# Performance work log

Hardware: AMD Instinct MI355X
Metric: run time of the kernel (lower is better)

## Reference

```python
import jax, jax.numpy as jnp
import numpy as np

DIM = 512
HEADS = 8
DIM_HEAD = 64
BLOCKS = 6
EXCHANGES = 3
EPS = 1.1920929e-07  # torch.finfo(float32).eps used by RMSNorm(eps=None)


def _rmsnorm(x, w):
    return x * jax.lax.rsqrt(jnp.mean(x * x, axis=-1, keepdims=True) + EPS) * w


def _attention(x, ctx, nw, wq, wkv, wo):
    # x: [B, i, d] queries; ctx: [B, j, d] context (NOT normalized, as in original)
    B = x.shape[0]
    xn = _rmsnorm(x, nw)
    q = jnp.einsum('bid,ed->bie', xn, wq)
    kv = jnp.einsum('bjd,ed->bje', ctx, wkv)
    k, v = jnp.split(kv, 2, axis=-1)
    heads = lambda t: t.reshape(B, t.shape[1], HEADS, DIM_HEAD).transpose(0, 2, 1, 3)
    q, k, v = heads(q), heads(k), heads(v)
    sim = jnp.einsum('bhid,bhjd->bhij', q, k)  # NOTE: original never applies self.scale
    attn = jax.nn.softmax(sim, axis=-1)
    out = jnp.einsum('bhij,bhjd->bhid', attn, v)
    out = out.transpose(0, 2, 1, 3).reshape(B, -1, HEADS * DIM_HEAD)
    return jnp.einsum('bie,de->bid', out, wo)


def _feedforward(x, nw, kw, kb, vw, vb):
    q = _rmsnorm(x, nw)
    h = jnp.einsum('...d,ed->...e', q, kw) + kb
    sim, gates = jnp.split(h, 2, axis=-1)
    h = sim * jax.nn.gelu(gates, approximate=False)  # F.gelu default = exact erf
    return jnp.einsum('...e,de->...d', h, vw) + vb


def _forward(tokens, attn_norm_w, attn_wq, attn_wkv, attn_wo,
             ff_norm_w, ff_keys_w, ff_keys_b, ff_values_w, ff_values_b,
             res_norm_w, res_wq, res_wkv, res_wo):
    b, n, d = tokens.shape
    tokens = jnp.broadcast_to(tokens[None], (BLOCKS, b, n, d))
    messages = [tokens]
    for _ in range(EXCHANGES):
        flat = tokens.reshape(BLOCKS * b, n, d)
        attended = _attention(flat, flat, attn_norm_w, attn_wq, attn_wkv, attn_wo)
        attended = attended.reshape(BLOCKS, b, n, d)
        retrieved = _feedforward(tokens, ff_norm_w, ff_keys_w, ff_keys_b, ff_values_w, ff_values_b)
        messages += [attended, retrieved]
        packed = jnp.concatenate(messages, axis=0)           # [M, b, n, d]
        M = packed.shape[0]
        # einops: repeat 'm b n d -> (b blocks) n m d'
        ctx = jnp.broadcast_to(packed.transpose(1, 2, 0, 3)[:, None], (b, BLOCKS, n, M, d))
        ctx = ctx.reshape(b * BLOCKS * n, M, d)
        # queries packed '(blocks b) n d' then '* n d' -> [blocks*b*n, 1, d]
        q = tokens.reshape(BLOCKS * b * n, 1, d)
        pooled = _attention(q, ctx, res_norm_w, res_wq, res_wkv, res_wo)
        tokens = pooled.reshape(BLOCKS, b, n, d)
    return tokens


def setup_inputs() -> dict:
    key = jax.random.key(0)
    ks = jax.random.split(key, 12)
    b, n, d = 2, 256, DIM
    di = HEADS * DIM_HEAD
    dff = int(d * 4.0 * 2 / 3)
    s = lambda k, shp, fan: (jax.random.normal(k, shp, jnp.float32) / np.sqrt(fan)).astype(jnp.float32)
    return {
        'tokens': jax.random.normal(ks[0], (b, n, d), jnp.float32),
        'attn_norm_w': 1.0 + 0.05 * jax.random.normal(ks[1], (d,), jnp.float32),
        'attn_wq': s(ks[2], (di, d), d),
        'attn_wkv': s(ks[3], (2 * di, d), d),
        'attn_wo': s(ks[4], (d, di), di),
        'ff_norm_w': 1.0 + 0.05 * jax.random.normal(ks[5], (d,), jnp.float32),
        'ff_keys_w': s(ks[6], (2 * dff, d), d),
        'ff_keys_b': 0.01 * jax.random.normal(ks[7], (2 * dff,), jnp.float32),
        'ff_values_w': s(ks[8], (d, dff), dff),
        'ff_values_b': 0.01 * jax.random.normal(ks[9], (d,), jnp.float32),
        'res_norm_w': 1.0 + 0.05 * jax.random.normal(ks[10], (d,), jnp.float32),
        'res_wq': s(ks[11], (di, d), d),
        'res_wkv': s(jax.random.fold_in(key, 100), (2 * di, d), d),
        'res_wo': s(jax.random.fold_in(key, 101), (d, di), di),
    }


def reference(tokens, attn_norm_w, attn_wq, attn_wkv, attn_wo,
              ff_norm_w, ff_keys_w, ff_keys_b, ff_values_w, ff_values_b,
              res_norm_w, res_wq, res_wkv, res_wo):
    return _forward(tokens, attn_norm_w, attn_wq, attn_wkv, attn_wo,
                    ff_norm_w, ff_keys_w, ff_keys_b, ff_values_w, ff_values_b,
                    res_norm_w, res_wq, res_wkv, res_wo)
```

## Files before the change

kernel.cpp:

```cpp
#include <hip/hip_runtime.h>
#include <math.h>

#define Dm   512
#define Nn_  256
#define Bv   2
#define NTD  1024
#define NH   8
#define DH   64
#define DFF  1365
#define DFF2 2730
#define KFF  1408
#define NFF  2816
#define NMD  14
#define EPSR 1.1920929e-07f

typedef _Float16 h16;
typedef h16  v8h  __attribute__((ext_vector_type(8)));
typedef float v4f __attribute__((ext_vector_type(4)));

__device__ inline h16 f2h(float v) { return (h16)v; }

__device__ inline void glds16(const void* g, void* l) {
    __builtin_amdgcn_global_load_lds((const __attribute__((address_space(1))) void*)g,
                                     (__attribute__((address_space(3))) void*)l, 16, 0, 0);
}

struct GDesc {
    const h16* A;
    const h16* W;
    const float* bias;
    const float* rss;
    float* C;
    h16* Cbf;
    long Apl, Wpl, bfpl;
    int lda, ldw, ldc, Nd, mbase, K, mode, nbx;
};

template <int BM, int BN>
__global__ __launch_bounds__(256) void mega_gemm(GDesc d0, GDesc d1, GDesc d2, GDesc d3,
                                                 int n0, int n01, int n012)
{
    constexpr int NWN = (BN == 128) ? 2 : 1;
    constexpr int NWM = 4 / NWN;
    constexpr int MI = BM / (16 * NWM);
    constexpr int ABUF = BM * 32;
    constexpr int WBUFh = BN * 32;
    constexpr int BUF = 2 * ABUF + 2 * WBUFh;
    constexpr int ASEG = BM / 16;
    constexpr int WSEG = BN / 16;
    constexpr int NSEG = 2 * ASEG + 2 * WSEG;
    __shared__ h16 lds[2 * BUF];

    GDesc d; int lb = blockIdx.x;
    if (lb < n0) d = d0;
    else if (lb < n01) { d = d1; lb -= n0; }
    else if (lb < n012) { d = d2; lb -= n01; }
    else { d = d3; lb -= n012; }
    const int bx = lb % d.nbx;
    const int by = lb / d.nbx;

    const int tid = threadIdx.x;
    const int wid = tid >> 6;
    const int lane = tid & 63;
    const int wm = wid / NWN, wn = wid % NWN;
    const int row16 = lane & 15, quad = lane >> 4;
    const long i0 = (long)bx * BM;
    const long j0 = (long)by * BN;
    const int l4 = lane >> 2;
    const int l2s = ((lane & 3) ^ (l4 & 3)) * 8;
    const int ksw = (quad ^ (row16 & 3)) * 8;

    auto stage = [&](int k0, h16* buf) {
        #pragma unroll
        for (int s = 0; s < NSEG / 4; ++s) {
            const int sg = wid * (NSEG / 4) + s;
            const h16* src;
            int dst;
            if (sg < ASEG) {
                src = d.A + (i0 + sg * 16 + l4) * (long)d.lda + k0 + l2s;
                dst = sg * 512;
            } else if (sg < 2 * ASEG) {
                const int r = sg - ASEG;
                src = d.A + d.Apl + (i0 + r * 16 + l4) * (long)d.lda + k0 + l2s;
                dst = ABUF + r * 512;
            } else if (sg < 2 * ASEG + WSEG) {
                const int r = sg - 2 * ASEG;
                src = d.W + (j0 + r * 16 + l4) * (long)d.ldw + k0 + l2s;
                dst = 2 * ABUF + r * 512;
            } else {
                const int r = sg - 2 * ASEG - WSEG;
                src = d.W + d.Wpl + (j0 + r * 16 + l4) * (long)d.ldw + k0 + l2s;
                dst = 2 * ABUF + WBUFh + r * 512;
            }
            glds16(src, &buf[dst]);
        }
    };

    v4f acc[MI][4];
    #pragma unroll
    for (int a = 0; a < MI; ++a)
        #pragma unroll
        for (int b = 0; b < 4; ++b) acc[a][b] = (v4f){0.f, 0.f, 0.f, 0.f};

    stage(0, lds);
    int cur = 0;
    for (int k0 = 0; k0 < d.K; k0 += 32) {
        __syncthreads();
        h16* cbuf = &lds[cur * BUF];
        if (k0 + 32 < d.K) stage(k0 + 32, &lds[(cur ^ 1) * BUF]);

        v8h af[MI], al[MI];
        #pragma unroll
        for (int mi = 0; mi < MI; ++mi) {
            const int aoff = (wm * (16 * MI) + mi * 16 + row16) * 32 + ksw;
            af[mi] = *(const v8h*)&cbuf[aoff];
            al[mi] = *(const v8h*)&cbuf[ABUF + aoff];
        }
        #pragma unroll
        for (int nj = 0; nj < 4; ++nj) {
            const int boff = (wn * 64 + nj * 16 + row16) * 32 + ksw;
            v8h bh = *(const v8h*)&cbuf[2 * ABUF + boff];
            v8h bl = *(const v8h*)&cbuf[2 * ABUF + WBUFh + boff];
            #pragma unroll
            for (int mi = 0; mi < MI; ++mi) {
                acc[mi][nj] = __builtin_amdgcn_mfma_f32_16x16x32_f16(af[mi], bh, acc[mi][nj], 0, 0, 0);
                acc[mi][nj] = __builtin_amdgcn_mfma_f32_16x16x32_f16(af[mi], bl, acc[mi][nj], 0, 0, 0);
                acc[mi][nj] = __builtin_amdgcn_mfma_f32_16x16x32_f16(al[mi], bh, acc[mi][nj], 0, 0, 0);
            }
        }
        cur ^= 1;
    }

    #pragma unroll
    for (int nj = 0; nj < 4; ++nj) {
        const int col = (int)j0 + wn * 64 + nj * 16 + row16;
        if (col < d.Nd) {
            const float bv = d.bias ? d.bias[col] : 0.f;
            #pragma unroll
            for (int mi = 0; mi < MI; ++mi) {
                #pragma unroll
                for (int r = 0; r < 4; ++r) {
                    const long row = i0 + wm * (16 * MI) + mi * 16 + quad * 4 + r;
                    float v = acc[mi][nj][r];
                    if (d.rss) v *= d.rss[(int)row];
                    v += bv;
                    if (d.mode == 0) {
                        d.C[row * (long)d.ldc + col] = v;
                    } else if (d.mode == 1) {
                        const long idx = row * (long)d.ldc + col;
                        const h16 hi = f2h(v);
                        d.Cbf[idx] = hi; d.Cbf[idx + d.bfpl] = f2h(v - (float)hi);
                    } else if (d.mode == 2) {
                        const long idx = row * (long)d.ldc + col;
                        d.C[idx] = v;
                        const h16 hi = f2h(v);
                        d.Cbf[idx] = hi; d.Cbf[idx + d.bfpl] = f2h(v - (float)hi);
                    } else if (d.mode == 3) {
                        const int rr = (int)row & 1023;
                        const int md = d.mbase * 2 + (rr >> 9);
                        const long orow = (long)(((rr >> 8) & 1) * 256 + (rr & 255)) * NMD + md;
                        d.C[orow * 1024 + col] = v;
                    } else if (d.mode == 4) {
                        const h16 hi = f2h(v);
                        const h16 lo = f2h(v - (float)hi);
                        if (col < 512) {
                            const long idx = row * 512 + col;
                            d.Cbf[idx] = hi; d.Cbf[idx + d.bfpl] = lo;
                        } else {
                            const int c = col - 512;
                            const int bh_ = ((int)(row >> 8)) * 8 + (c >> 6);
                            const long idx = (((long)bh_ * 64 + (c & 63)) << 8) + (row & 255);
                            h16* vtp = (h16*)d.C;
                            vtp[idx] = hi; vtp[idx + d.bfpl] = lo;
                        }
                    } else {
                        const int g = (int)(row >> 9), bb = ((int)row >> 8) & 1, nn = (int)row & 255;
                        #pragma unroll
                        for (int rep = 0; rep < 3; ++rep) {
                            const long orow = (long)(((g * 3 + rep) * 2 + bb) * 256 + nn);
                            d.C[orow * (long)d.ldc + col] = v;
                        }
                    }
                }
            }
        }
    }
}

struct SetupP {
    const float *attn_wq, *attn_wkv, *ff_keys_w, *res_wq, *res_wkv, *res_wo,
                *attn_wo, *ff_values_w, *ff_values_b,
                *attn_norm_w, *ff_norm_w, *res_norm_w, *tok_in;
    h16 *wqb, *wkvb, *fkb, *rqb, *rkvb, *rob, *woTb, *fvwTb, *tokbf;
    float *biasWf, *tokens;
};

__device__ inline void cvt_dev(int idx, const float* x, int Ms, int Ks, int Kp,
                               h16* y, long plane, const float* cs)
{
    const int row = idx / Kp;
    const int col = idx - row * Kp;
    float v = (row < Ms && col < Ks) ? x[(long)row * Ks + col] : 0.f;
    if (cs) v *= cs[col];
    const h16 hi = f2h(v);
    y[idx] = hi;
    y[idx + plane] = f2h(v - (float)hi);
}

__device__ inline void cvtT_dev(int idx, const float* x, int R, int C,
                                h16* y, long plane)
{
    const int row = idx / R;
    const int col = idx - row * R;
    const float v = (row < C) ? x[(long)col * C + row] : 0.f;
    const h16 hi = f2h(v);
    y[idx] = hi;
    y[idx + plane] = f2h(v - (float)hi);
}

__global__ __launch_bounds__(256) void setup_all(SetupP p)
{
    long b = blockIdx.x;
    const int t = threadIdx.x;
    if (b < 1024) { cvt_dev((int)(b * 256 + t), p.attn_wq, 512, 512, 512, p.wqb, 512L * 512, p.attn_norm_w); return; }
    b -= 1024;
    if (b < 2048) { cvt_dev((int)(b * 256 + t), p.attn_wkv, 1024, 512, 512, p.wkvb, 1024L * 512, nullptr); return; }
    b -= 2048;
    if (b < 5632) { cvt_dev((int)(b * 256 + t), p.ff_keys_w, DFF2, 512, 512, p.fkb, (long)NFF * 512, p.ff_norm_w); return; }
    b -= 5632;
    if (b < 1024) { cvt_dev((int)(b * 256 + t), p.res_wq, 512, 512, 512, p.rqb, 512L * 512, p.res_norm_w); return; }
    b -= 1024;
    if (b < 2048) { cvt_dev((int)(b * 256 + t), p.res_wkv, 1024, 512, 512, p.rkvb, 1024L * 512, nullptr); return; }
    b -= 2048;
    if (b < 1024) { cvt_dev((int)(b * 256 + t), p.res_wo, 512, 512, 512, p.rob, 512L * 512, nullptr); return; }
    b -= 1024;
    if (b < 1024) { cvtT_dev((int)(b * 256 + t), p.attn_wo, 512, 512, p.woTb, 512L * 512); return; }
    b -= 1024;
    if (b < 2816) { cvtT_dev((int)(b * 256 + t), p.ff_values_w, 512, DFF, p.fvwTb, (long)KFF * 512); return; }
    b -= 2816;
    if (b < 4) {
        const int n = (int)(b * 256 + t);
        if (n < 1024) {
            float s = 0.f;
            const float* row = p.res_wkv + (long)n * 512;
            for (int dd = 0; dd < 512; ++dd) s = fmaf(row[dd], p.ff_values_b[dd], s);
            p.biasWf[n] = s;
        }
        return;
    }
    b -= 4;
    {
        const int idx = (int)(b * 256 + t);
        const float v = p.tok_in[idx & (Bv * Nn_ * Dm - 1)];
        p.tokens[idx] = v;
        const h16 hi = f2h(v);
        p.tokbf[idx] = hi;
        p.tokbf[idx + (long)NTD * Dm] = f2h(v - (float)hi);
    }
}
#define SETUP_BLOCKS 18692

__global__ __launch_bounds__(256) void rs_kernel(const float* __restrict__ x,
                                                 float* __restrict__ rs)
{
    const int r = blockIdx.x * 4 + (threadIdx.x >> 6);
    const int lane = threadIdx.x & 63;
    const float* row = x + (long)r * Dm + lane * 8;
    float ss = 0.f;
    #pragma unroll
    for (int i = 0; i < 8; i += 4) {
        const float4 v = *(const float4*)(row + i);
        ss += v.x * v.x + v.y * v.y + v.z * v.z + v.w * v.w;
    }
    #pragma unroll
    for (int off = 32; off > 0; off >>= 1) ss += __shfl_xor(ss, off, 64);
    if (lane == 0) rs[r] = rsqrtf(ss * (1.f / 512.f) + EPSR);
}

__global__ __launch_bounds__(256) void attn_glu(
    const h16* __restrict__ qhl, const h16* __restrict__ khl,
    const h16* __restrict__ vtb, long pl, h16* __restrict__ outbf,
    const float* __restrict__ hbuf, h16* __restrict__ hbf, long hpl)
{
    if (blockIdx.x >= 128) {
        const int r = blockIdx.x - 128;
        const float* row = hbuf + (long)r * NFF;
        for (int c = threadIdx.x; c < KFF; c += 256) {
            float v = 0.f;
            if (c < DFF) {
                const float sim = row[c];
                const float g = row[c + DFF];
                v = sim * (0.5f * g * (1.f + erff(g * 0.70710678118654752440f)));
            }
            const long idx = (long)r * KFF + c;
            const h16 hi = f2h(v);
            hbf[idx] = hi;
            hbf[idx + hpl] = f2h(v - (float)hi);
        }
        return;
    }

    __shared__ h16 kh[4096], kl[4096], vh[4096], vl[4096];
    __shared__ h16 pH[4 * 1024], pL[4 * 1024];

    const int bat = blockIdx.x >> 5;
    const int head = (blockIdx.x >> 2) & 7;
    const int qc = blockIdx.x & 3;
    const int t = threadIdx.x;
    const int w = t >> 6, lane = t & 63;
    const int row16 = lane & 15, quad = lane >> 4;

    v8h qh[2], ql[2];
    {
        const long qrow = (long)bat * 256 + qc * 64 + w * 16 + row16;
        const h16* qp = qhl + qrow * 512 + head * 64 + quad * 8;
        qh[0] = *(const v8h*)qp;        qh[1] = *(const v8h*)(qp + 32);
        ql[0] = *(const v8h*)(qp + pl); ql[1] = *(const v8h*)(qp + pl + 32);
    }

    v4f O[4];
    #pragma unroll
    for (int i = 0; i < 4; ++i) O[i] = (v4f){0.f, 0.f, 0.f, 0.f};
    float m[4] = {-1e30f, -1e30f, -1e30f, -1e30f};
    float l[4] = {0.f, 0.f, 0.f, 0.f};

    const int sj = t >> 3;
    const int sc = t & 7;
    const long kbase = ((long)bat * 256) * 512 + head * 64;
    const long vbase = ((long)(bat * 8 + head) * 64) << 8;

    for (int jc = 0; jc < 256; jc += 64) {
        __syncthreads();
        #pragma unroll
        for (int rep = 0; rep < 2; ++rep) {
            const int row = sj + rep * 32;
            const int dsw = row * 64 + ((sc ^ (row & 7)) * 8);
            const h16* ks = khl + kbase + (long)(jc + row) * 512 + sc * 8;
            const h16* vs = vtb + vbase + ((long)row << 8) + jc + sc * 8;
            *(v8h*)&kh[dsw] = *(const v8h*)ks;
            *(v8h*)&kl[dsw] = *(const v8h*)(ks + pl);
            *(v8h*)&vh[dsw] = *(const v8h*)vs;
            *(v8h*)&vl[dsw] = *(const v8h*)(vs + pl);
        }
        __syncthreads();

        v4f S[4];
        #pragma unroll
        for (int i = 0; i < 4; ++i) S[i] = (v4f){0.f, 0.f, 0.f, 0.f};
        #pragma unroll
        for (int kk = 0; kk < 2; ++kk) {
            #pragma unroll
            for (int tile = 0; tile < 4; ++tile) {
                const int off = (tile * 16 + row16) * 64 + (((kk * 4 + quad) ^ (row16 & 7)) * 8);
                v8h bh = *(const v8h*)&kh[off];
                v8h bl = *(const v8h*)&kl[off];
                S[tile] = __builtin_amdgcn_mfma_f32_16x16x32_f16(qh[kk], bh, S[tile], 0, 0, 0);
                S[tile] = __builtin_amdgcn_mfma_f32_16x16x32_f16(qh[kk], bl, S[tile], 0, 0, 0);
                S[tile] = __builtin_amdgcn_mfma_f32_16x16x32_f16(ql[kk], bh, S[tile], 0, 0, 0);
            }
        }

        float mc[4], sums[4], alpha[4];
        #pragma unroll
        for (int r = 0; r < 4; ++r) {
            float v = fmaxf(fmaxf(S[0][r], S[1][r]), fmaxf(S[2][r], S[3][r]));
            v = fmaxf(v, __shfl_xor(v, 1, 64));
            v = fmaxf(v, __shfl_xor(v, 2, 64));
            v = fmaxf(v, __shfl_xor(v, 4, 64));
            v = fmaxf(v, __shfl_xor(v, 8, 64));
            mc[r] = v;
        }
        #pragma unroll
        for (int r = 0; r < 4; ++r) {
            const float mn = fmaxf(m[r], mc[r]);
            alpha[r] = __expf(m[r] - mn);
            m[r] = mn;
            sums[r] = 0.f;
        }
        #pragma unroll
        for (int tile = 0; tile < 4; ++tile) {
            #pragma unroll
            for (int r = 0; r < 4; ++r) {
                const float p = __expf(S[tile][r] - m[r]);
                S[tile][r] = p;
                sums[r] += p;
            }
        }
        #pragma unroll
        for (int r = 0; r < 4; ++r) {
            float v = sums[r];
            v += __shfl_xor(v, 1, 64);
            v += __shfl_xor(v, 2, 64);
            v += __shfl_xor(v, 4, 64);
            v += __shfl_xor(v, 8, 64);
            l[r] = l[r] * alpha[r] + v;
        }
        #pragma unroll
        for (int tile = 0; tile < 4; ++tile)
            #pragma unroll
            for (int r = 0; r < 4; ++r) O[tile][r] *= alpha[r];

        #pragma unroll
        for (int tile = 0; tile < 4; ++tile) {
            const int chunkcol = tile * 2 + (row16 >> 3);
            #pragma unroll
            for (int r = 0; r < 4; ++r) {
                const int prow = quad * 4 + r;
                const int addr = w * 1024 + prow * 64 +
                                 ((chunkcol ^ (prow & 7)) * 8) + (row16 & 7);
                const float p = S[tile][r];
                const h16 hi = f2h(p);
                pH[addr] = hi;
                pL[addr] = f2h(p - (float)hi);
            }
        }

        #pragma unroll
        for (int kk = 0; kk < 2; ++kk) {
            const int poff = w * 1024 + row16 * 64 + (((kk * 4 + quad) ^ (row16 & 7)) * 8);
            v8h pa = *(const v8h*)&pH[poff];
            v8h pb = *(const v8h*)&pL[poff];
            #pragma unroll
            for (int tile = 0; tile < 4; ++tile) {
                const int off = (tile * 16 + row16) * 64 + (((kk * 4 + quad) ^ (row16 & 7)) * 8);
                v8h vbh = *(const v8h*)&vh[off];
                v8h vbl = *(const v8h*)&vl[off];
                O[tile] = __builtin_amdgcn_mfma_f32_16x16x32_f16(pa, vbh, O[tile], 0, 0, 0);
                O[tile] = __builtin_amdgcn_mfma_f32_16x16x32_f16(pa, vbl, O[tile], 0, 0, 0);
                O[tile] = __builtin_amdgcn_mfma_f32_16x16x32_f16(pb, vbh, O[tile], 0, 0, 0);
            }
        }
    }

    #pragma unroll
    for (int tile = 0; tile < 4; ++tile) {
        const int dim = tile * 16 + row16;
        #pragma unroll
        for (int r = 0; r < 4; ++r) {
            const long grow = (long)bat * 256 + qc * 64 + w * 16 + quad * 4 + r;
            const float v = O[tile][r] / l[r];
            const long idx = grow * 512 + head * 64 + dim;
            const h16 hi = f2h(v);
            outbf[idx] = hi;
            outbf[idx + pl] = f2h(v - (float)hi);
        }
    }
}

template <int M>
__global__ __launch_bounds__(128) void attn_pool_kernel(
    const float* __restrict__ qb, const float* __restrict__ kvc3,
    h16* __restrict__ outbf, long plane)
{
    const int rb = blockIdx.x >> 3;
    const int h = blockIdx.x & 7;
    __shared__ float k_lds[M * 66];
    __shared__ float v_lds[M * 66];
    __shared__ float q_lds[2 * 64];
    __shared__ float p_lds[2 * 64];
    const int t = threadIdx.x;
    const int g = rb >> 8, nn = rb & 255;

    for (int idx = t; idx < M * 64; idx += 128) {
        const int m = idx >> 6, d = idx & 63;
        const long base = ((long)rb * NMD + m) * 1024 + h * DH + d;
        k_lds[m * 66 + d] = kvc3[base];
        v_lds[m * 66 + d] = kvc3[base + 512];
    }
    {
        const int w = t >> 6, dd = t & 63;
        const long iq = (long)(g * 2 + w) * 256 + nn;
        q_lds[t] = qb[iq * Dm + h * DH + dd];
    }
    __syncthreads();

    const int w = t >> 6;
    const int lane = t & 63;
    float s = -1e30f;
    if (lane < M) {
        s = 0.f;
        const float* kr = &k_lds[lane * 66];
        const float* qr = &q_lds[w * 64];
        #pragma unroll
        for (int dd = 0; dd < 64; dd += 2) {
            s = fmaf(qr[dd], kr[dd], s);
            s = fmaf(qr[dd + 1], kr[dd + 1], s);
        }
    }
    float mx = s;
    #pragma unroll
    for (int off = 32; off > 0; off >>= 1) mx = fmaxf(mx, __shfl_xor(mx, off, 64));
    const float p = __expf(s - mx);
    float l = p;
    #pragma unroll
    for (int off = 32; off > 0; off >>= 1) l += __shfl_xor(l, off, 64);
    p_lds[w * 64 + lane] = p / l;

    float o = 0.f;
    const float* pr = &p_lds[w * 64];
    #pragma unroll
    for (int m = 0; m < M; ++m)
        o = fmaf(pr[m], v_lds[m * 66 + lane], o);

    const long iq = (long)(g * 2 + w) * 256 + nn;
    const long oidx = iq * Dm + h * DH + lane;
    const h16 hi = f2h(o);
    outbf[oidx] = hi;
    outbf[oidx + plane] = f2h(o - (float)hi);
}

extern "C" void kernel_launch(void* const* d_in, const int* in_sizes, int n_in,
                              void* d_out, int out_size, void* d_ws, size_t ws_size,
                              hipStream_t stream)
{
    const float* tok_in       = (const float*)d_in[0];
    const float* attn_norm_w  = (const float*)d_in[1];
    const float* attn_wq      = (const float*)d_in[2];
    const float* attn_wkv     = (const float*)d_in[3];
    const float* attn_wo      = (const float*)d_in[4];
    const float* ff_norm_w    = (const float*)d_in[5];
    const float* ff_keys_w    = (const float*)d_in[6];
    const float* ff_keys_b    = (const float*)d_in[7];
    const float* ff_values_w  = (const float*)d_in[8];
    const float* ff_values_b  = (const float*)d_in[9];
    const float* res_norm_w   = (const float*)d_in[10];
    const float* res_wq       = (const float*)d_in[11];
    const float* res_wkv      = (const float*)d_in[12];
    const float* res_wo       = (const float*)d_in[13];

    float* ws = (float*)d_ws;
    float* kvc3   = ws;
    float* tokens = kvc3 + 512L * NMD * 1024;
    float* qbuf   = tokens + (long)NTD * Dm;
    float* hbuf   = qbuf + (long)NTD * Dm;
    float* biasWf = hbuf + (long)NTD * NFF;
    float* rsbuf  = biasWf + 1024;

    h16* us = (h16*)(rsbuf + 1024);
    const long apl = (long)NTD * Dm;
    const long hpl = (long)NTD * KFF;
    const long w1 = 512L * 512, w2 = 1024L * 512, w3 = (long)NFF * 512;
    const long w5 = (long)KFF * 512;
    const long wa_pl = 1024L * 512;
    const long wf_pl = 1024L * KFF;
    h16* tokbf = us; us += 2 * apl;
    h16* abf   = us; us += 2 * apl;
    h16* hbf   = us; us += 2 * hpl;
    h16* qhl   = us; us += 2 * apl;
    h16* khl   = us; us += 2 * apl;
    h16* vtb   = us; us += 2 * apl;
    h16* wqb   = us; us += 2 * w1;
    h16* wkvb  = us; us += 2 * w2;
    h16* fkb   = us; us += 2 * w3;
    h16* rqb   = us; us += 2 * w1;
    h16* rkvb  = us; us += 2 * w2;
    h16* rob   = us; us += 2 * w1;
    h16* woTb  = us; us += 2 * w1;
    h16* fvwTb = us; us += 2 * w5;
    h16* Wab   = us; us += 2 * wa_pl;
    h16* Wfb   = us; us += 2 * wf_pl;

    {
        SetupP p;
        p.attn_wq = attn_wq; p.attn_wkv = attn_wkv; p.ff_keys_w = ff_keys_w;
        p.res_wq = res_wq; p.res_wkv = res_wkv; p.res_wo = res_wo;
        p.attn_wo = attn_wo; p.ff_values_w = ff_values_w; p.ff_values_b = ff_values_b;
        p.attn_norm_w = attn_norm_w; p.ff_norm_w = ff_norm_w; p.res_norm_w = res_norm_w;
        p.tok_in = tok_in;
        p.wqb = wqb; p.wkvb = wkvb; p.fkb = fkb; p.rqb = rqb; p.rkvb = rkvb;
        p.rob = rob; p.woTb = woTb; p.fvwTb = fvwTb; p.tokbf = tokbf;
        p.biasWf = biasWf; p.tokens = tokens;
        setup_all<<<SETUP_BLOCKS, 256, 0, stream>>>(p);
    }

    auto mk = [](const h16* A, long Apl, int lda,
                 const h16* W, long Wpl, int ldw,
                 const float* bias, const float* rss,
                 float* C, int ldc, int Nd,
                 h16* Cbf, long bfpl, int mbase, int K,
                 int mode, int nbx) -> GDesc {
        GDesc d;
        d.A = A; d.Apl = Apl; d.lda = lda;
        d.W = W; d.Wpl = Wpl; d.ldw = ldw;
        d.bias = bias; d.rss = rss; d.C = C; d.ldc = ldc; d.Nd = Nd;
        d.Cbf = Cbf; d.bfpl = bfpl; d.mbase = mbase; d.K = K;
        d.mode = mode; d.nbx = nbx;
        return d;
    };

    {
        GDesc dWf = mk(rkvb, w2, 512, fvwTb, w5, 512, nullptr, nullptr, nullptr, KFF, KFF,
                       Wfb, wf_pl, 0, 512, 1, 16);
        GDesc dWa = mk(rkvb, w2, 512, woTb, w1, 512, nullptr, nullptr, nullptr, 512, 512,
                       Wab, wa_pl, 0, 512, 1, 16);
        mega_gemm<64, 64><<<480, 256, 0, stream>>>(dWf, dWa, dWa, dWa, 352, 480, 480);
    }

    for (int e = 0; e < 3; ++e) {
        rs_kernel<<<256, 256, 0, stream>>>(tokens, rsbuf);
        {
            GDesc dffk = mk(tokbf, apl, 512, fkb,  w3, 512, ff_keys_b, rsbuf, hbuf, NFF, DFF2,
                            nullptr, 0, 0, 512, 0, 16);
            GDesc dwkv = mk(tokbf, apl, 512, wkvb, w2, 512, nullptr, nullptr, (float*)vtb, 1024, 1024,
                            khl, apl, 0, 512, 4, 16);
            GDesc dwq  = mk(tokbf, apl, 512, wqb,  w1, 512, nullptr, rsbuf, nullptr, 512, 512,
                            qhl, apl, 0, 512, 1, 16);
            mega_gemm<64, 64><<<1088, 256, 0, stream>>>(dffk, dwkv, dwq, dwq, 704, 960, 1088);
        }
        attn_glu<<<1152, 256, 0, stream>>>(qhl, khl, vtb, apl, abf, hbuf, hbf, hpl);
        {
            GDesc dffvKV = mk(hbf, hpl, KFF, Wfb, wf_pl, KFF, biasWf, nullptr, kvc3, 1024, 1024,
                              nullptr, 0, 2 + 2 * e, KFF, 3, 16);
            GDesc dwoKV  = mk(abf, apl, 512, Wab, wa_pl, 512, nullptr, nullptr, kvc3, 1024, 1024,
                              nullptr, 0, 1 + 2 * e, 512, 3, 16);
            GDesc drq    = mk(tokbf, apl, 512, rqb, w1, 512, nullptr, rsbuf, qbuf, 512, 512,
                              nullptr, 0, 0, 512, 0, 16);
            if (e == 0) {
                GDesc dtokKV = mk(tokbf, apl, 512, rkvb, w2, 512, nullptr, nullptr, kvc3, 1024, 1024,
                                  nullptr, 0, 0, 512, 3, 16);
                mega_gemm<64, 64><<<896, 256, 0, stream>>>(dffvKV, dwoKV, drq, dtokKV, 256, 512, 640);
            } else {
                mega_gemm<64, 64><<<640, 256, 0, stream>>>(dffvKV, dwoKV, drq, drq, 256, 512, 640);
            }
        }
        if (e == 0)      attn_pool_kernel<6><<<512 * NH, 128, 0, stream>>>(qbuf, kvc3, abf, apl);
        else if (e == 1) attn_pool_kernel<10><<<512 * NH, 128, 0, stream>>>(qbuf, kvc3, abf, apl);
        else             attn_pool_kernel<14><<<512 * NH, 128, 0, stream>>>(qbuf, kvc3, abf, apl);
        {
            if (e < 2) {
                GDesc dro = mk(abf, apl, 512, rob, w1, 512, nullptr, nullptr, tokens, 512, 512,
                               tokbf, apl, 0, 512, 2, 32);
                mega_gemm<32, 128><<<128, 256, 0, stream>>>(dro, dro, dro, dro, 128, 128, 128);
            } else {
                GDesc dro = mk(abf, apl, 512, rob, w1, 512, nullptr, nullptr, (float*)d_out, 512, 512,
                               nullptr, 0, 0, 512, 5, 32);
                mega_gemm<32, 128><<<128, 256, 0, stream>>>(dro, dro, dro, dro, 128, 128, 128);
            }
        }
    }
}
```

Measured before the change: 467.0 us.

## Fuse GEGLU into ff-keys GEMM epilogue and rebalance GEMM launches

Interleaves the ff_keys weight rows (sim, gate pairs) at setup so that each gate column sits next to its sim column, then computes GELU gating inside the GEMM epilogue via a lane shuffle. The GEGLU result is written directly as hi/lo fp16. This removes the fp32 hbuf intermediate and the separate GLU blocks in the attention kernel. The res-query GEMM moves into the first mega-GEMM launch and the token KV projection moves into the one-time weight-prep launch, shrinking the later per-exchange launch. The cost is extra erf work in the epilogue, where half of the lanes sit idle.

```diff
diff --git a/kernel.cpp b/kernel.cpp
--- a/kernel.cpp
+++ b/kernel.cpp
@@ -173,13 +173,22 @@
                             h16* vtp = (h16*)d.C;
                             vtp[idx] = hi; vtp[idx + d.bfpl] = lo;
                         }
-                    } else {
+                    } else if (d.mode == 5) {
                         const int g = (int)(row >> 9), bb = ((int)row >> 8) & 1, nn = (int)row & 255;
                         #pragma unroll
                         for (int rep = 0; rep < 3; ++rep) {
                             const long orow = (long)(((g * 3 + rep) * 2 + bb) * 256 + nn);
                             d.C[orow * (long)d.ldc + col] = v;
                         }
+                    } else {
+                        const float gt = __shfl_xor(v, 1, 64);
+                        if ((col & 1) == 0) {
+                            const float ge = 0.5f * gt * (1.f + erff(gt * 0.70710678118654752440f));
+                            const float out = v * ge;
+                            const long idx = row * (long)d.ldc + (col >> 1);
+                            const h16 hi = f2h(out);
+                            d.Cbf[idx] = hi; d.Cbf[idx + d.bfpl] = f2h(out - (float)hi);
+                        }
                     }
                 }
             }
@@ -188,11 +197,11 @@
 }
 
 struct SetupP {
-    const float *attn_wq, *attn_wkv, *ff_keys_w, *res_wq, *res_wkv, *res_wo,
-                *attn_wo, *ff_values_w, *ff_values_b,
+    const float *attn_wq, *attn_wkv, *ff_keys_w, *ff_keys_b, *res_wq, *res_wkv,
+                *res_wo, *attn_wo, *ff_values_w, *ff_values_b,
                 *attn_norm_w, *ff_norm_w, *res_norm_w, *tok_in;
     h16 *wqb, *wkvb, *fkb, *rqb, *rkvb, *rob, *woTb, *fvwTb, *tokbf;
-    float *biasWf, *tokens;
+    float *biasWf, *biasFK, *tokens;
 };
 
 __device__ inline void cvt_dev(int idx, const float* x, int Ms, int Ks, int Kp,
@@ -226,8 +235,19 @@
     b -= 1024;
     if (b < 2048) { cvt_dev((int)(b * 256 + t), p.attn_wkv, 1024, 512, 512, p.wkvb, 1024L * 512, nullptr); return; }
     b -= 2048;
-    if (b < 5632) { cvt_dev((int)(b * 256 + t), p.ff_keys_w, DFF2, 512, 512, p.fkb, (long)NFF * 512, p.ff_norm_w); return; }
-    b -= 5632;
+    if (b < 5504) {
+        const int idx = (int)(b * 256 + t);
+        const int rr = idx >> 9, col = idx & 511;
+        const int i = rr >> 1;
+        const int src = (rr & 1) ? i + DFF : i;
+        float v = 0.f;
+        if (i < DFF) v = p.ff_keys_w[(long)src * 512 + col] * p.ff_norm_w[col];
+        const h16 hi = f2h(v);
+        p.fkb[idx] = hi;
+        p.fkb[idx + (long)NFF * 512] = f2h(v - (float)hi);
+        return;
+    }
+    b -= 5504;
     if (b < 1024) { cvt_dev((int)(b * 256 + t), p.res_wq, 512, 512, 512, p.rqb, 512L * 512, p.res_norm_w); return; }
     b -= 1024;
     if (b < 2048) { cvt_dev((int)(b * 256 + t), p.res_wkv, 1024, 512, 512, p.rkvb, 1024L * 512, nullptr); return; }
@@ -249,6 +269,16 @@
         return;
     }
     b -= 4;
+    if (b < 11) {
+        const int rr = (int)(b * 256 + t);
+        if (rr < 2752) {
+            const int i = rr >> 1;
+            const int src = (rr & 1) ? i + DFF : i;
+            p.biasFK[rr] = (i < DFF) ? p.ff_keys_b[src] : 0.f;
+        }
+        return;
+    }
+    b -= 11;
     {
         const int idx = (int)(b * 256 + t);
         const float v = p.tok_in[idx & (Bv * Nn_ * Dm - 1)];
@@ -258,7 +288,7 @@
         p.tokbf[idx + (long)NTD * Dm] = f2h(v - (float)hi);
     }
 }
-#define SETUP_BLOCKS 18692
+#define SETUP_BLOCKS 18575
 
 __global__ __launch_bounds__(256) void rs_kernel(const float* __restrict__ x,
                                                  float* __restrict__ rs)
@@ -277,29 +307,10 @@
     if (lane == 0) rs[r] = rsqrtf(ss * (1.f / 512.f) + EPSR);
 }
 
-__global__ __launch_bounds__(256) void attn_glu(
+__global__ __launch_bounds__(256) void attn_self_mfma(
     const h16* __restrict__ qhl, const h16* __restrict__ khl,
-    const h16* __restrict__ vtb, long pl, h16* __restrict__ outbf,
-    const float* __restrict__ hbuf, h16* __restrict__ hbf, long hpl)
-{
-    if (blockIdx.x >= 128) {
-        const int r = blockIdx.x - 128;
-        const float* row = hbuf + (long)r * NFF;
-        for (int c = threadIdx.x; c < KFF; c += 256) {
-            float v = 0.f;
-            if (c < DFF) {
-                const float sim = row[c];
-                const float g = row[c + DFF];
-                v = sim * (0.5f * g * (1.f + erff(g * 0.70710678118654752440f)));
-            }
-            const long idx = (long)r * KFF + c;
-            const h16 hi = f2h(v);
-            hbf[idx] = hi;
-            hbf[idx + hpl] = f2h(v - (float)hi);
-        }
-        return;
-    }
-
+    const h16* __restrict__ vtb, long pl, h16* __restrict__ outbf)
+{
     __shared__ h16 kh[4096], kl[4096], vh[4096], vl[4096];
     __shared__ h16 pH[4 * 1024], pL[4 * 1024];
 
@@ -532,9 +543,9 @@
     float* kvc3   = ws;
     float* tokens = kvc3 + 512L * NMD * 1024;
     float* qbuf   = tokens + (long)NTD * Dm;
-    float* hbuf   = qbuf + (long)NTD * Dm;
-    float* biasWf = hbuf + (long)NTD * NFF;
-    float* rsbuf  = biasWf + 1024;
+    float* biasWf = qbuf + (long)NTD * Dm;
+    float* biasFK = biasWf + 1024;
+    float* rsbuf  = biasFK + 2752;
 
     h16* us = (h16*)(rsbuf + 1024);
     const long apl = (long)NTD * Dm;
@@ -563,13 +574,14 @@
     {
         SetupP p;
         p.attn_wq = attn_wq; p.attn_wkv = attn_wkv; p.ff_keys_w = ff_keys_w;
-        p.res_wq = res_wq; p.res_wkv = res_wkv; p.res_wo = res_wo;
-        p.attn_wo = attn_wo; p.ff_values_w = ff_values_w; p.ff_values_b = ff_values_b;
+        p.ff_keys_b = ff_keys_b; p.res_wq = res_wq; p.res_wkv = res_wkv;
+        p.res_wo = res_wo; p.attn_wo = attn_wo; p.ff_values_w = ff_values_w;
+        p.ff_values_b = ff_values_b;
         p.attn_norm_w = attn_norm_w; p.ff_norm_w = ff_norm_w; p.res_norm_w = res_norm_w;
         p.tok_in = tok_in;
         p.wqb = wqb; p.wkvb = wkvb; p.fkb = fkb; p.rqb = rqb; p.rkvb = rkvb;
         p.rob = rob; p.woTb = woTb; p.fvwTb = fvwTb; p.tokbf = tokbf;
-        p.biasWf = biasWf; p.tokens = tokens;
+        p.biasWf = biasWf; p.biasFK = biasFK; p.tokens = tokens;
         setup_all<<<SETUP_BLOCKS, 256, 0, stream>>>(p);
     }
 
@@ -593,35 +605,31 @@
                        Wfb, wf_pl, 0, 512, 1, 16);
         GDesc dWa = mk(rkvb, w2, 512, woTb, w1, 512, nullptr, nullptr, nullptr, 512, 512,
                        Wab, wa_pl, 0, 512, 1, 16);
-        mega_gemm<64, 64><<<480, 256, 0, stream>>>(dWf, dWa, dWa, dWa, 352, 480, 480);
+        GDesc dtokKV = mk(tokbf, apl, 512, rkvb, w2, 512, nullptr, nullptr, kvc3, 1024, 1024,
+                          nullptr, 0, 0, 512, 3, 16);
+        mega_gemm<64, 64><<<736, 256, 0, stream>>>(dWf, dWa, dtokKV, dtokKV, 352, 480, 736);
     }
 
     for (int e = 0; e < 3; ++e) {
         rs_kernel<<<256, 256, 0, stream>>>(tokens, rsbuf);
         {
-            GDesc dffk = mk(tokbf, apl, 512, fkb,  w3, 512, ff_keys_b, rsbuf, hbuf, NFF, DFF2,
-                            nullptr, 0, 0, 512, 0, 16);
+            GDesc dffk = mk(tokbf, apl, 512, fkb,  w3, 512, biasFK, rsbuf, nullptr, KFF, DFF2,
+                            hbf, hpl, 0, 512, 6, 16);
             GDesc dwkv = mk(tokbf, apl, 512, wkvb, w2, 512, nullptr, nullptr, (float*)vtb, 1024, 1024,
                             khl, apl, 0, 512, 4, 16);
             GDesc dwq  = mk(tokbf, apl, 512, wqb,  w1, 512, nullptr, rsbuf, nullptr, 512, 512,
                             qhl, apl, 0, 512, 1, 16);
-            mega_gemm<64, 64><<<1088, 256, 0, stream>>>(dffk, dwkv, dwq, dwq, 704, 960, 1088);
-        }
-        attn_glu<<<1152, 256, 0, stream>>>(qhl, khl, vtb, apl, abf, hbuf, hbf, hpl);
+            GDesc drq  = mk(tokbf, apl, 512, rqb,  w1, 512, nullptr, rsbuf, qbuf, 512, 512,
+                            nullptr, 0, 0, 512, 0, 16);
+            mega_gemm<64, 64><<<1200, 256, 0, stream>>>(dffk, dwkv, dwq, drq, 688, 944, 1072);
+        }
+        attn_self_mfma<<<128, 256, 0, stream>>>(qhl, khl, vtb, apl, abf);
         {
             GDesc dffvKV = mk(hbf, hpl, KFF, Wfb, wf_pl, KFF, biasWf, nullptr, kvc3, 1024, 1024,
                               nullptr, 0, 2 + 2 * e, KFF, 3, 16);
             GDesc dwoKV  = mk(abf, apl, 512, Wab, wa_pl, 512, nullptr, nullptr, kvc3, 1024, 1024,
                               nullptr, 0, 1 + 2 * e, 512, 3, 16);
-            GDesc drq    = mk(tokbf, apl, 512, rqb, w1, 512, nullptr, rsbuf, qbuf, 512, 512,
-                              nullptr, 0, 0, 512, 0, 16);
-            if (e == 0) {
-                GDesc dtokKV = mk(tokbf, apl, 512, rkvb, w2, 512, nullptr, nullptr, kvc3, 1024, 1024,
-                                  nullptr, 0, 0, 512, 3, 16);
-                mega_gemm<64, 64><<<896, 256, 0, stream>>>(dffvKV, dwoKV, drq, dtokKV, 256, 512, 640);
-            } else {
-                mega_gemm<64, 64><<<640, 256, 0, stream>>>(dffvKV, dwoKV, drq, drq, 256, 512, 640);
-            }
+            mega_gemm<64, 64><<<512, 256, 0, stream>>>(dffvKV, dwoKV, dwoKV, dwoKV, 256, 512, 512);
         }
         if (e == 0)      attn_pool_kernel<6><<<512 * NH, 128, 0, stream>>>(qbuf, kvc3, abf, apl);
         else if (e == 1) attn_pool_kernel<10><<<512 * NH, 128, 0, stream>>>(qbuf, kvc3, abf, apl);
```

Result: no change. 474.9 us (+1.7%).
